# Kernel tuning notes

Measured on AMD Instinct MI355X. Metric: run time of the kernel, lower is better.

## Reference

```python
import jax, jax.numpy as jnp
import numpy as np

B, S, C, H, W = 8, 64, 3, 224, 224   # batch, n_segments, channels, height, width
E, P = 128, 16                        # embed_dim, patch size of feature extractor


def _conv(x, w, b, stride, padding):
    y = jax.lax.conv_general_dilated(
        x, w, (stride, stride), padding,
        dimension_numbers=('NCHW', 'OIHW', 'NCHW'))
    return y + b[None, :, None, None]


def setup_inputs() -> dict:
    key = jax.random.key(0)
    k1, k2, k3 = jax.random.split(key, 3)
    img = jax.random.normal(k1, (B, C, H, W), jnp.float32)
    # SpixelNet stand-in: 3x3 conv -> n_segments logit channels
    w_spixel = jax.random.normal(k2, (S, C, 3, 3), jnp.float32) * 0.1
    b_spixel = jnp.zeros((S,), jnp.float32)
    # feature extractor stand-in: 16x16/16 patch conv -> embed_dim, then GAP
    w_patch = jax.random.normal(k3, (E, C, P, P), jnp.float32) * 0.02
    b_patch = jnp.zeros((E,), jnp.float32)
    return dict(img=img, w_spixel=w_spixel, b_spixel=b_spixel,
                w_patch=w_patch, b_patch=b_patch)


def reference(img, w_spixel, b_spixel, w_patch, b_patch):
    # superpixel tokenizer -> segment logits, argmax -> hard labels
    logits = _conv(img, w_spixel, b_spixel, 1, 'SAME')          # [B,S,H,W]
    labels = jnp.argmax(logits, axis=1)                          # [B,H,W] int

    # replicate per-batch torch.unique (sorted unique labels, zero-padded)
    flat = labels.reshape(B, -1)
    present = jnp.zeros((B, S), bool).at[jnp.arange(B)[:, None], flat].set(True)
    vals = jnp.where(present, jnp.arange(S)[None, :], S)
    uniq = jnp.sort(vals, axis=1)                                # uniques first
    uniq = jnp.where(uniq < S, uniq, 0)                          # pad with 0 like torch.zeros

    # broadcast-compare mask build + masked extract (the memory-bound op)
    mask = (labels[:, None, :, :] == uniq[:, :, None, None]).astype(img.dtype)  # [B,S,H,W]
    seg = (img[:, None, :, :, :] * mask[:, :, None, :, :]).reshape(B * S, C, H, W)

    # feature extractor: patch conv + global average pool
    feat = _conv(seg, w_patch, b_patch, P, 'VALID')              # [B*S,E,H/P,W/P]
    feat = feat.mean(axis=(2, 3))                                # [B*S,E]
    return feat.reshape(B, S, E)
```

## Files before the change

### kernel.cpp

```cpp
#include <hip/hip_runtime.h>

#define BD 8
#define SD 64
#define CD 3
#define HD 224
#define WD 224
#define ED 128
#define PD 16
#define HWD (HD*WD)
#define KD (CD*PD*PD)
#define PRT 8
#define CHK (HWD/PRT)

__device__ float              g_part[BD * CD * PRT * SD * 256];
__device__ float              g_buf[BD * SD * KD];
__device__ int                g_labels[BD * HWD];
__device__ unsigned long long g_ppres[BD * PRT];

__global__ __launch_bounds__(256) void k_labels(
    const float* __restrict__ img,
    const float* __restrict__ wsp,
    const float* __restrict__ bsp)
{
    const int w = blockIdx.x * 64 + threadIdx.x;
    const int h = blockIdx.y * 4 + threadIdx.y;
    const int b = blockIdx.z;
    if (w >= WD) return;

    const float* ib = img + (size_t)b * CD * HWD;
    float pix[27];
    #pragma unroll
    for (int c = 0; c < 3; ++c)
        #pragma unroll
        for (int dh = 0; dh < 3; ++dh)
            #pragma unroll
            for (int dw = 0; dw < 3; ++dw) {
                int hh = h + dh - 1, ww = w + dw - 1;
                bool ok = (hh >= 0) & (hh < HD) & (ww >= 0) & (ww < WD);
                pix[(c * 3 + dh) * 3 + dw] = ok ? ib[c * HWD + hh * WD + ww] : 0.f;
            }

    float best = -INFINITY;
    int bi = 0;
    for (int s = 0; s < SD; ++s) {
        const float* wr = wsp + s * 27;
        float acc = bsp[s];
        #pragma unroll
        for (int j = 0; j < 27; ++j) acc = fmaf(pix[j], wr[j], acc);
        if (acc > best) { best = acc; bi = s; }
    }
    g_labels[b * HWD + h * WD + w] = bi;
}

__global__ __launch_bounds__(256) void k_hist(const float* __restrict__ img)
{
    const int part = blockIdx.x, c = blockIdx.y, b = blockIdx.z;
    const int tid = threadIdx.x;

    __shared__ float acc[SD * 256];
    __shared__ unsigned long long pm;
    #pragma unroll
    for (int k = 0; k < 16; ++k)
        ((float4*)acc)[k * 256 + tid] = make_float4(0.f, 0.f, 0.f, 0.f);
    if (tid == 0) pm = 0ull;
    __syncthreads();

    const int start = part * CHK;
    const int*   lb = g_labels + (size_t)b * HWD;
    const float* ic = img + ((size_t)b * CD + c) * HWD;

    unsigned long long m = 0ull;
    for (int p = start + tid; p < start + CHK; p += 256) {
        const int lab = lb[p];
        const int h = p / WD, w = p - h * WD;
        const int cell = ((h & 15) << 4) | (w & 15);
        atomicAdd(&acc[lab * 256 + cell], ic[p]);
        m |= 1ull << lab;
    }
    #pragma unroll
    for (int d = 1; d < 64; d <<= 1) m |= __shfl_xor(m, d, 64);
    if ((tid & 63) == 0) atomicOr(&pm, m);
    __syncthreads();

    float4* dst = (float4*)(g_part + (((size_t)(b * CD + c)) * PRT + part) * (SD * 256));
    #pragma unroll
    for (int k = 0; k < 16; ++k)
        dst[k * 256 + tid] = ((float4*)acc)[k * 256 + tid];
    if (c == 0 && tid == 0) g_ppres[b * PRT + part] = pm;
}

__global__ __launch_bounds__(256) void k_merge()
{
    const int t = blockIdx.x * 256 + threadIdx.x;
    const int cell4 = t & 63;
    int q = t >> 6;
    const int c = q % 3; q /= 3;
    const int lab = q & 63;
    const int b = q >> 6;

    const float4* src = (const float4*)g_part
        + ((size_t)(b * CD + c) * PRT) * 4096 + lab * 64 + cell4;
    float4 s = src[0];
    #pragma unroll
    for (int p2 = 1; p2 < PRT; ++p2) {
        float4 v = src[(size_t)p2 * 4096];
        s.x += v.x; s.y += v.y; s.z += v.z; s.w += v.w;
    }
    ((float4*)g_buf)[t] = s;
}

__global__ __launch_bounds__(256) void k_out(
    const float* __restrict__ wp,
    const float* __restrict__ bp,
    float* __restrict__ out)
{
    const int i = blockIdx.x;
    const int b = blockIdx.y;
    const int lane = threadIdx.x & 63;
    const int wv = threadIdx.x >> 6;

    unsigned long long m = 0ull;
    #pragma unroll
    for (int p2 = 0; p2 < PRT; ++p2) m |= g_ppres[b * PRT + p2];

    int l = 0;
    if (i < __popcll(m)) {
        unsigned long long mm = m;
        for (int t = 0; t < i; ++t) mm &= mm - 1;
        l = __builtin_ctzll(mm);
    }

    const float4* gr = (const float4*)(g_buf + (size_t)(b * SD + l) * KD);
    const float4 g0 = gr[lane], g1 = gr[lane + 64], g2 = gr[lane + 128];

    #pragma unroll 4
    for (int j = 0; j < 32; ++j) {
        const int e = wv * 32 + j;
        const float4* wr = (const float4*)(wp + (size_t)e * KD);
        float4 a0 = wr[lane], a1 = wr[lane + 64], a2 = wr[lane + 128];
        float acc = g0.x * a0.x;
        acc = fmaf(g0.y, a0.y, acc); acc = fmaf(g0.z, a0.z, acc); acc = fmaf(g0.w, a0.w, acc);
        acc = fmaf(g1.x, a1.x, acc); acc = fmaf(g1.y, a1.y, acc);
        acc = fmaf(g1.z, a1.z, acc); acc = fmaf(g1.w, a1.w, acc);
        acc = fmaf(g2.x, a2.x, acc); acc = fmaf(g2.y, a2.y, acc);
        acc = fmaf(g2.z, a2.z, acc); acc = fmaf(g2.w, a2.w, acc);
        #pragma unroll
        for (int off = 32; off; off >>= 1) acc += __shfl_xor(acc, off, 64);
        if (lane == 0)
            out[(size_t)(b * SD + i) * ED + e] = bp[e] + acc * (1.f / 196.f);
    }
}

extern "C" void kernel_launch(void* const* d_in, const int* in_sizes, int n_in,
                              void* d_out, int out_size, void* d_ws, size_t ws_size,
                              hipStream_t stream) {
    const float *img = nullptr, *wsp = nullptr, *bsp = nullptr, *wp = nullptr, *bp = nullptr;
    for (int i = 0; i < n_in; ++i) {
        switch (in_sizes[i]) {
            case BD * CD * HWD:      img = (const float*)d_in[i]; break;
            case SD * CD * 9:        wsp = (const float*)d_in[i]; break;
            case SD:                 bsp = (const float*)d_in[i]; break;
            case ED * CD * PD * PD:  wp  = (const float*)d_in[i]; break;
            case ED:                 bp  = (const float*)d_in[i]; break;
        }
    }
    float* out = (float*)d_out;

    dim3 b1(64, 4, 1), g1(4, 56, BD);
    k_labels<<<g1, b1, 0, stream>>>(img, wsp, bsp);

    dim3 g2(PRT, CD, BD);
    k_hist<<<g2, 256, 0, stream>>>(img);

    k_merge<<<384, 256, 0, stream>>>();

    dim3 g4(SD, BD, 1);
    k_out<<<g4, 256, 0, stream>>>(wp, bp, out);
}
```

Before: 135.6 us.

## Register-block 4 rows per thread in label conv and fuse merge into output kernel

The label kernel now has each thread compute four vertically adjacent pixels. It reuses a sliding 6x3 input window per channel, which cuts redundant global loads and amortizes the weight reads across pixels, and the grid shrinks to match. The separate merge kernel is removed. Each output block now sums the partial histograms for its own label directly into shared memory, which saves a launch and the g_buf round trip. The cost is that partial sums for padded duplicate labels (label 0) get recomputed, and k_labels launches fewer blocks with more registers per thread.

```diff
diff --git a/kernel.cpp b/kernel.cpp
--- a/kernel.cpp
+++ b/kernel.cpp
@@ -11,9 +11,9 @@
 #define KD (CD*PD*PD)
 #define PRT 8
 #define CHK (HWD/PRT)
+#define PIX 4
 
 __device__ float              g_part[BD * CD * PRT * SD * 256];
-__device__ float              g_buf[BD * SD * KD];
 __device__ int                g_labels[BD * HWD];
 __device__ unsigned long long g_ppres[BD * PRT];
 
@@ -22,34 +22,56 @@
     const float* __restrict__ wsp,
     const float* __restrict__ bsp)
 {
-    const int w = blockIdx.x * 64 + threadIdx.x;
-    const int h = blockIdx.y * 4 + threadIdx.y;
-    const int b = blockIdx.z;
+    const int w  = blockIdx.x * 64 + threadIdx.x;
+    const int h0 = (blockIdx.y * 4 + threadIdx.y) * PIX;
+    const int b  = blockIdx.z;
     if (w >= WD) return;
 
     const float* ib = img + (size_t)b * CD * HWD;
-    float pix[27];
+    float win[CD][PIX + 2][3];
     #pragma unroll
-    for (int c = 0; c < 3; ++c)
+    for (int c = 0; c < CD; ++c)
         #pragma unroll
-        for (int dh = 0; dh < 3; ++dh)
+        for (int r = 0; r < PIX + 2; ++r) {
+            const int hh = h0 + r - 1;
+            const bool okh = (hh >= 0) & (hh < HD);
             #pragma unroll
-            for (int dw = 0; dw < 3; ++dw) {
-                int hh = h + dh - 1, ww = w + dw - 1;
-                bool ok = (hh >= 0) & (hh < HD) & (ww >= 0) & (ww < WD);
-                pix[(c * 3 + dh) * 3 + dw] = ok ? ib[c * HWD + hh * WD + ww] : 0.f;
+            for (int d = 0; d < 3; ++d) {
+                const int ww = w + d - 1;
+                const bool ok = okh & (ww >= 0) & (ww < WD);
+                win[c][r][d] = ok ? ib[c * HWD + hh * WD + ww] : 0.f;
             }
+        }
 
-    float best = -INFINITY;
-    int bi = 0;
+    float best[PIX];
+    int   lab[PIX];
+    #pragma unroll
+    for (int p = 0; p < PIX; ++p) { best[p] = -INFINITY; lab[p] = 0; }
+
     for (int s = 0; s < SD; ++s) {
         const float* wr = wsp + s * 27;
-        float acc = bsp[s];
+        const float  bv = bsp[s];
+        float acc[PIX];
         #pragma unroll
-        for (int j = 0; j < 27; ++j) acc = fmaf(pix[j], wr[j], acc);
-        if (acc > best) { best = acc; bi = s; }
+        for (int p = 0; p < PIX; ++p) acc[p] = bv;
+        #pragma unroll
+        for (int c = 0; c < CD; ++c)
+            #pragma unroll
+            for (int dh = 0; dh < 3; ++dh)
+                #pragma unroll
+                for (int dw = 0; dw < 3; ++dw) {
+                    const float wt = wr[c * 9 + dh * 3 + dw];
+                    #pragma unroll
+                    for (int p = 0; p < PIX; ++p)
+                        acc[p] = fmaf(win[c][p + dh][dw], wt, acc[p]);
+                }
+        #pragma unroll
+        for (int p = 0; p < PIX; ++p)
+            if (acc[p] > best[p]) { best[p] = acc[p]; lab[p] = s; }
     }
-    g_labels[b * HWD + h * WD + w] = bi;
+    #pragma unroll
+    for (int p = 0; p < PIX; ++p)
+        g_labels[b * HWD + (h0 + p) * WD + w] = lab[p];
 }
 
 __global__ __launch_bounds__(256) void k_hist(const float* __restrict__ img)
@@ -89,35 +111,17 @@
     if (c == 0 && tid == 0) g_ppres[b * PRT + part] = pm;
 }
 
-__global__ __launch_bounds__(256) void k_merge()
-{
-    const int t = blockIdx.x * 256 + threadIdx.x;
-    const int cell4 = t & 63;
-    int q = t >> 6;
-    const int c = q % 3; q /= 3;
-    const int lab = q & 63;
-    const int b = q >> 6;
-
-    const float4* src = (const float4*)g_part
-        + ((size_t)(b * CD + c) * PRT) * 4096 + lab * 64 + cell4;
-    float4 s = src[0];
-    #pragma unroll
-    for (int p2 = 1; p2 < PRT; ++p2) {
-        float4 v = src[(size_t)p2 * 4096];
-        s.x += v.x; s.y += v.y; s.z += v.z; s.w += v.w;
-    }
-    ((float4*)g_buf)[t] = s;
-}
-
 __global__ __launch_bounds__(256) void k_out(
     const float* __restrict__ wp,
     const float* __restrict__ bp,
     float* __restrict__ out)
 {
+    __shared__ float4 gs4[KD / 4];
     const int i = blockIdx.x;
     const int b = blockIdx.y;
-    const int lane = threadIdx.x & 63;
-    const int wv = threadIdx.x >> 6;
+    const int tid = threadIdx.x;
+    const int lane = tid & 63;
+    const int wv = tid >> 6;
 
     unsigned long long m = 0ull;
     #pragma unroll
@@ -130,8 +134,21 @@
         l = __builtin_ctzll(mm);
     }
 
-    const float4* gr = (const float4*)(g_buf + (size_t)(b * SD + l) * KD);
-    const float4 g0 = gr[lane], g1 = gr[lane + 64], g2 = gr[lane + 128];
+    if (tid < KD / 4) {
+        const int c = tid >> 6, cell4 = tid & 63;
+        const float4* src = (const float4*)g_part
+            + ((size_t)(b * CD + c) * PRT) * 4096 + l * 64 + cell4;
+        float4 s = src[0];
+        #pragma unroll
+        for (int p2 = 1; p2 < PRT; ++p2) {
+            float4 v = src[(size_t)p2 * 4096];
+            s.x += v.x; s.y += v.y; s.z += v.z; s.w += v.w;
+        }
+        gs4[tid] = s;
+    }
+    __syncthreads();
+
+    const float4 g0 = gs4[lane], g1 = gs4[lane + 64], g2 = gs4[lane + 128];
 
     #pragma unroll 4
     for (int j = 0; j < 32; ++j) {
@@ -166,14 +183,12 @@
     }
     float* out = (float*)d_out;
 
-    dim3 b1(64, 4, 1), g1(4, 56, BD);
+    dim3 b1(64, 4, 1), g1(4, 14, BD);
     k_labels<<<g1, b1, 0, stream>>>(img, wsp, bsp);
 
     dim3 g2(PRT, CD, BD);
     k_hist<<<g2, 256, 0, stream>>>(img);
 
-    k_merge<<<384, 256, 0, stream>>>();
-
-    dim3 g4(SD, BD, 1);
-    k_out<<<g4, 256, 0, stream>>>(wp, bp, out);
+    dim3 g3(SD, BD, 1);
+    k_out<<<g3, 256, 0, stream>>>(wp, bp, out);
 }
```

Result: slower. 138.6 us (+2.3%).

## Fuse partial-histogram merge into output GEMV and process four segments per block

Applied to the files above, without the earlier changes.

Removes the separate merge kernel and its global staging buffer. Each output block now sums the per-partition partial histograms for its selected segments straight into shared memory, then reuses every loaded weight row across four segments. This saves one launch and a global round trip, and cuts repeated weight reads. In exchange there are fewer blocks (128 instead of 512), so parallelism drops, and padded duplicate segments may merge the same data more than once.

```diff
diff --git a/kernel.cpp b/kernel.cpp
--- a/kernel.cpp
+++ b/kernel.cpp
@@ -13,7 +13,6 @@
 #define CHK (HWD/PRT)
 
 __device__ float              g_part[BD * CD * PRT * SD * 256];
-__device__ float              g_buf[BD * SD * KD];
 __device__ int                g_labels[BD * HWD];
 __device__ unsigned long long g_ppres[BD * PRT];
 
@@ -89,65 +88,71 @@
     if (c == 0 && tid == 0) g_ppres[b * PRT + part] = pm;
 }
 
-__global__ __launch_bounds__(256) void k_merge()
-{
-    const int t = blockIdx.x * 256 + threadIdx.x;
-    const int cell4 = t & 63;
-    int q = t >> 6;
-    const int c = q % 3; q /= 3;
-    const int lab = q & 63;
-    const int b = q >> 6;
-
-    const float4* src = (const float4*)g_part
-        + ((size_t)(b * CD + c) * PRT) * 4096 + lab * 64 + cell4;
-    float4 s = src[0];
-    #pragma unroll
-    for (int p2 = 1; p2 < PRT; ++p2) {
-        float4 v = src[(size_t)p2 * 4096];
-        s.x += v.x; s.y += v.y; s.z += v.z; s.w += v.w;
-    }
-    ((float4*)g_buf)[t] = s;
-}
-
 __global__ __launch_bounds__(256) void k_out(
     const float* __restrict__ wp,
     const float* __restrict__ bp,
     float* __restrict__ out)
 {
-    const int i = blockIdx.x;
-    const int b = blockIdx.y;
-    const int lane = threadIdx.x & 63;
-    const int wv = threadIdx.x >> 6;
+    __shared__ float4 gs4[4][KD / 4];
+    const int i0 = blockIdx.x * 4;
+    const int b  = blockIdx.y;
+    const int tid = threadIdx.x;
+    const int lane = tid & 63;
+    const int wv = tid >> 6;
 
     unsigned long long m = 0ull;
     #pragma unroll
     for (int p2 = 0; p2 < PRT; ++p2) m |= g_ppres[b * PRT + p2];
+    const int npres = __popcll(m);
 
-    int l = 0;
-    if (i < __popcll(m)) {
-        unsigned long long mm = m;
-        for (int t = 0; t < i; ++t) mm &= mm - 1;
-        l = __builtin_ctzll(mm);
+    int lsel[4];
+    #pragma unroll
+    for (int ii = 0; ii < 4; ++ii) {
+        int l = 0;
+        if (i0 + ii < npres) {
+            unsigned long long mm = m;
+            for (int t = 0; t < i0 + ii; ++t) mm &= mm - 1;
+            l = __builtin_ctzll(mm);
+        }
+        lsel[ii] = l;
     }
 
-    const float4* gr = (const float4*)(g_buf + (size_t)(b * SD + l) * KD);
-    const float4 g0 = gr[lane], g1 = gr[lane + 64], g2 = gr[lane + 128];
+    #pragma unroll
+    for (int r = 0; r < 3; ++r) {
+        const int t = r * 256 + tid;
+        const int ii = t / 192, k4 = t - ii * 192;
+        const int c = k4 >> 6, cell4 = k4 & 63;
+        const float4* src = (const float4*)g_part
+            + ((size_t)(b * CD + c) * PRT) * 4096 + lsel[ii] * 64 + cell4;
+        float4 s = src[0];
+        #pragma unroll
+        for (int p2 = 1; p2 < PRT; ++p2) {
+            float4 v = src[(size_t)p2 * 4096];
+            s.x += v.x; s.y += v.y; s.z += v.z; s.w += v.w;
+        }
+        gs4[ii][k4] = s;
+    }
+    __syncthreads();
 
-    #pragma unroll 4
+    #pragma unroll 2
     for (int j = 0; j < 32; ++j) {
         const int e = wv * 32 + j;
         const float4* wr = (const float4*)(wp + (size_t)e * KD);
-        float4 a0 = wr[lane], a1 = wr[lane + 64], a2 = wr[lane + 128];
-        float acc = g0.x * a0.x;
-        acc = fmaf(g0.y, a0.y, acc); acc = fmaf(g0.z, a0.z, acc); acc = fmaf(g0.w, a0.w, acc);
-        acc = fmaf(g1.x, a1.x, acc); acc = fmaf(g1.y, a1.y, acc);
-        acc = fmaf(g1.z, a1.z, acc); acc = fmaf(g1.w, a1.w, acc);
-        acc = fmaf(g2.x, a2.x, acc); acc = fmaf(g2.y, a2.y, acc);
-        acc = fmaf(g2.z, a2.z, acc); acc = fmaf(g2.w, a2.w, acc);
+        const float4 a0 = wr[lane], a1 = wr[lane + 64], a2 = wr[lane + 128];
         #pragma unroll
-        for (int off = 32; off; off >>= 1) acc += __shfl_xor(acc, off, 64);
-        if (lane == 0)
-            out[(size_t)(b * SD + i) * ED + e] = bp[e] + acc * (1.f / 196.f);
+        for (int ii = 0; ii < 4; ++ii) {
+            const float4 g0 = gs4[ii][lane], g1 = gs4[ii][lane + 64], g2 = gs4[ii][lane + 128];
+            float acc = g0.x * a0.x;
+            acc = fmaf(g0.y, a0.y, acc); acc = fmaf(g0.z, a0.z, acc); acc = fmaf(g0.w, a0.w, acc);
+            acc = fmaf(g1.x, a1.x, acc); acc = fmaf(g1.y, a1.y, acc);
+            acc = fmaf(g1.z, a1.z, acc); acc = fmaf(g1.w, a1.w, acc);
+            acc = fmaf(g2.x, a2.x, acc); acc = fmaf(g2.y, a2.y, acc);
+            acc = fmaf(g2.z, a2.z, acc); acc = fmaf(g2.w, a2.w, acc);
+            #pragma unroll
+            for (int off = 32; off; off >>= 1) acc += __shfl_xor(acc, off, 64);
+            if (lane == 0)
+                out[(size_t)(b * SD + i0 + ii) * ED + e] = bp[e] + acc * (1.f / 196.f);
+        }
     }
 }
 
@@ -172,8 +177,6 @@
     dim3 g2(PRT, CD, BD);
     k_hist<<<g2, 256, 0, stream>>>(img);
 
-    k_merge<<<384, 256, 0, stream>>>();
-
-    dim3 g4(SD, BD, 1);
-    k_out<<<g4, 256, 0, stream>>>(wp, bp, out);
+    dim3 g3(SD / 4, BD, 1);
+    k_out<<<g3, 256, 0, stream>>>(wp, bp, out);
 }
```

Result: slower. 153.5 us (+13.2%).

## Fuse partial-histogram merge into output kernel and flatten label grid

Applied to the files above, without the earlier changes.

Removes the separate merge kernel and its intermediate buffer. Each output block now sums the per-part partial histograms for its label into shared memory before the dot products. The label kernel switches to a flat 1D pixel indexing, so no threads are wasted on the 224-wide rows. This costs redundant merge reads when several blocks map to the same (padded) label.

```diff
diff --git a/kernel.cpp b/kernel.cpp
--- a/kernel.cpp
+++ b/kernel.cpp
@@ -13,7 +13,6 @@
 #define CHK (HWD/PRT)
 
 __device__ float              g_part[BD * CD * PRT * SD * 256];
-__device__ float              g_buf[BD * SD * KD];
 __device__ int                g_labels[BD * HWD];
 __device__ unsigned long long g_ppres[BD * PRT];
 
@@ -22,10 +21,10 @@
     const float* __restrict__ wsp,
     const float* __restrict__ bsp)
 {
-    const int w = blockIdx.x * 64 + threadIdx.x;
-    const int h = blockIdx.y * 4 + threadIdx.y;
-    const int b = blockIdx.z;
-    if (w >= WD) return;
+    const int p = blockIdx.x * 256 + threadIdx.x;
+    const int b = blockIdx.y;
+    const int h = p / WD;
+    const int w = p - h * WD;
 
     const float* ib = img + (size_t)b * CD * HWD;
     float pix[27];
@@ -49,7 +48,7 @@
         for (int j = 0; j < 27; ++j) acc = fmaf(pix[j], wr[j], acc);
         if (acc > best) { best = acc; bi = s; }
     }
-    g_labels[b * HWD + h * WD + w] = bi;
+    g_labels[b * HWD + p] = bi;
 }
 
 __global__ __launch_bounds__(256) void k_hist(const float* __restrict__ img)
@@ -89,35 +88,17 @@
     if (c == 0 && tid == 0) g_ppres[b * PRT + part] = pm;
 }
 
-__global__ __launch_bounds__(256) void k_merge()
-{
-    const int t = blockIdx.x * 256 + threadIdx.x;
-    const int cell4 = t & 63;
-    int q = t >> 6;
-    const int c = q % 3; q /= 3;
-    const int lab = q & 63;
-    const int b = q >> 6;
-
-    const float4* src = (const float4*)g_part
-        + ((size_t)(b * CD + c) * PRT) * 4096 + lab * 64 + cell4;
-    float4 s = src[0];
-    #pragma unroll
-    for (int p2 = 1; p2 < PRT; ++p2) {
-        float4 v = src[(size_t)p2 * 4096];
-        s.x += v.x; s.y += v.y; s.z += v.z; s.w += v.w;
-    }
-    ((float4*)g_buf)[t] = s;
-}
-
 __global__ __launch_bounds__(256) void k_out(
     const float* __restrict__ wp,
     const float* __restrict__ bp,
     float* __restrict__ out)
 {
+    __shared__ float4 gs4[KD / 4];
     const int i = blockIdx.x;
     const int b = blockIdx.y;
-    const int lane = threadIdx.x & 63;
-    const int wv = threadIdx.x >> 6;
+    const int tid = threadIdx.x;
+    const int lane = tid & 63;
+    const int wv = tid >> 6;
 
     unsigned long long m = 0ull;
     #pragma unroll
@@ -130,8 +111,21 @@
         l = __builtin_ctzll(mm);
     }
 
-    const float4* gr = (const float4*)(g_buf + (size_t)(b * SD + l) * KD);
-    const float4 g0 = gr[lane], g1 = gr[lane + 64], g2 = gr[lane + 128];
+    if (tid < KD / 4) {
+        const int c = tid >> 6, cell4 = tid & 63;
+        const float4* src = (const float4*)g_part
+            + ((size_t)(b * CD + c) * PRT) * 4096 + l * 64 + cell4;
+        float4 s = src[0];
+        #pragma unroll
+        for (int p2 = 1; p2 < PRT; ++p2) {
+            float4 v = src[(size_t)p2 * 4096];
+            s.x += v.x; s.y += v.y; s.z += v.z; s.w += v.w;
+        }
+        gs4[tid] = s;
+    }
+    __syncthreads();
+
+    const float4 g0 = gs4[lane], g1 = gs4[lane + 64], g2 = gs4[lane + 128];
 
     #pragma unroll 4
     for (int j = 0; j < 32; ++j) {
@@ -166,14 +160,12 @@
     }
     float* out = (float*)d_out;
 
-    dim3 b1(64, 4, 1), g1(4, 56, BD);
-    k_labels<<<g1, b1, 0, stream>>>(img, wsp, bsp);
+    dim3 g1(HWD / 256, BD, 1);
+    k_labels<<<g1, 256, 0, stream>>>(img, wsp, bsp);
 
     dim3 g2(PRT, CD, BD);
     k_hist<<<g2, 256, 0, stream>>>(img);
 
-    k_merge<<<384, 256, 0, stream>>>();
-
-    dim3 g4(SD, BD, 1);
-    k_out<<<g4, 256, 0, stream>>>(wp, bp, out);
+    dim3 g3(SD, BD, 1);
+    k_out<<<g3, 256, 0, stream>>>(wp, bp, out);
 }
```

New measurement: 134.0 us. About the same (-1.2%).
